# Kernel optimization log

Hardware: AMD Instinct MI355X
Metric: run time of the kernel (lower is better)

The kernel has to match this reference:

```python
import jax, jax.numpy as jnp
import numpy as np

# irreps_in = 128x0e + 64x1o + 32x2e -> (multiplicity, 2l+1) blocks
IRREPS = [(128, 1), (64, 3), (32, 5)]
DIM = sum(m * d for m, d in IRREPS)  # 480
EPS = 1e-8


def setup_inputs() -> dict:
    key = jax.random.key(0)
    features = jax.random.normal(key, (100000, DIM), dtype=jnp.float32)
    return {"features": features}


def reference(features) -> jnp.ndarray:
    batch = features.shape[:-1]
    out_blocks = []
    off = 0
    for mul, d in IRREPS:  # fixed small structural loop over irrep types
        block = features[..., off:off + mul * d].reshape(*batch, mul, d)
        # per-irrep L2 norm over the (2l+1) components -> (..., mul)
        norms = jnp.sqrt(jnp.sum(block * block, axis=-1))
        eps_norms = jnp.maximum(norms, EPS)
        scalings = jax.nn.silu(eps_norms) / eps_norms
        out_blocks.append((block * scalings[..., None]).reshape(*batch, mul * d))
        off += mul * d
    return jnp.concatenate(out_blocks, axis=-1)
```

## Files before the change

kernel.cpp:

```cpp
#include <hip/hip_runtime.h>
#include <math.h>

#define DIM 480
#define ROWS 8
#define BLOCK 64
#define NLOADS 15

typedef float f4 __attribute__((ext_vector_type(4)));

__device__ __forceinline__ float sig_of(float n) {
    n = fmaxf(n, 1e-8f);
    return __builtin_amdgcn_rcpf(1.0f + __expf(-n));
}

template <int R>
__device__ __forceinline__ void scale_groups(float* sbuf, int lane) {
    #pragma unroll
    for (int k = 0; k < R / 2; ++k) {
        const int a4 = k * 64 + lane;
        f4* p = (f4*)(sbuf + (a4 >> 5) * DIM) + (a4 & 31);
        f4 x = *p;
        x.x *= sig_of(fabsf(x.x));
        x.y *= sig_of(fabsf(x.y));
        x.z *= sig_of(fabsf(x.z));
        x.w *= sig_of(fabsf(x.w));
        *p = x;
    }
    #pragma unroll
    for (int k = 0; k < R; ++k) {
        const int b = k * 64 + lane;
        float* p = sbuf + (b >> 6) * DIM + 128 + 3 * (b & 63);
        const float x0 = p[0], x1 = p[1], x2 = p[2];
        const float s = sig_of(sqrtf(x0*x0 + x1*x1 + x2*x2));
        p[0] = x0 * s; p[1] = x1 * s; p[2] = x2 * s;
    }
    #pragma unroll
    for (int k = 0; k < R / 2; ++k) {
        const int c = k * 64 + lane;
        float* p = sbuf + (c >> 5) * DIM + 320 + 5 * (c & 31);
        const float x0 = p[0], x1 = p[1], x2 = p[2], x3 = p[3], x4 = p[4];
        const float s = sig_of(sqrtf(x0*x0 + x1*x1 + x2*x2 + x3*x3 + x4*x4));
        p[0] = x0*s; p[1] = x1*s; p[2] = x2*s; p[3] = x3*s; p[4] = x4*s;
    }
}

__device__ void scale_groups_rt(float* sbuf, int lane, int rows) {
    for (int a = lane; a < rows * 128; a += 64) {
        float* p = sbuf + (a >> 7) * DIM + (a & 127);
        const float x = *p;
        *p = x * sig_of(fabsf(x));
    }
    for (int b = lane; b < rows * 64; b += 64) {
        float* p = sbuf + (b >> 6) * DIM + 128 + 3 * (b & 63);
        const float x0 = p[0], x1 = p[1], x2 = p[2];
        const float s = sig_of(sqrtf(x0*x0 + x1*x1 + x2*x2));
        p[0] = x0 * s; p[1] = x1 * s; p[2] = x2 * s;
    }
    for (int c = lane; c < rows * 32; c += 64) {
        float* p = sbuf + (c >> 5) * DIM + 320 + 5 * (c & 31);
        const float x0 = p[0], x1 = p[1], x2 = p[2], x3 = p[3], x4 = p[4];
        const float s = sig_of(sqrtf(x0*x0 + x1*x1 + x2*x2 + x3*x3 + x4*x4));
        p[0] = x0*s; p[1] = x1*s; p[2] = x2*s; p[3] = x3*s; p[4] = x4*s;
    }
}

__global__ __launch_bounds__(BLOCK) void norm_act_kernel(
    const float* __restrict__ in, float* __restrict__ out, int n_rows)
{
    __shared__ __align__(16) float sbuf[ROWS * DIM];
    const int lane = threadIdx.x;
    const int row0 = blockIdx.x * ROWS;
    const int rows = min(ROWS, n_rows - row0);

    const float* gsrc = in  + (size_t)row0 * DIM;
    float*       gdst = out + (size_t)row0 * DIM;

    if (rows == ROWS) {
        #pragma unroll
        for (int k = 0; k < NLOADS; ++k) {
            const float* gp = gsrc + (size_t)(k * 64 + lane) * 4;
            __builtin_amdgcn_global_load_lds(
                (const __attribute__((address_space(1))) void*)gp,
                (__attribute__((address_space(3))) void*)((char*)sbuf + k * 1024),
                16, 0, 0);
        }
        asm volatile("s_waitcnt vmcnt(0)" ::: "memory");

        scale_groups<ROWS>(sbuf, lane);

        #pragma unroll
        for (int k = 0; k < NLOADS; ++k) {
            const int v = k * 64 + lane;
            __builtin_nontemporal_store(((const f4*)sbuf)[v], (f4*)gdst + v);
        }
    } else if (rows > 0) {
        for (int v = lane; v < rows * (DIM / 4); v += BLOCK)
            ((f4*)sbuf)[v] = ((const f4*)gsrc)[v];
        scale_groups_rt(sbuf, lane, rows);
        for (int v = lane; v < rows * (DIM / 4); v += BLOCK)
            __builtin_nontemporal_store(((const f4*)sbuf)[v], (f4*)gdst + v);
    }
}

extern "C" void kernel_launch(void* const* d_in, const int* in_sizes, int n_in,
                              void* d_out, int out_size, void* d_ws, size_t ws_size,
                              hipStream_t stream) {
    const float* in  = (const float*)d_in[0];
    float*       out = (float*)d_out;
    const int n_rows = in_sizes[0] / DIM;
    const int grid   = (n_rows + ROWS - 1) / ROWS;
    norm_act_kernel<<<grid, BLOCK, 0, stream>>>(in, out, n_rows);
}
```

Measured before the change: 324.2 us.

## Use persistent blocks with register double-buffered tile prefetch

Replaces the one-block-per-tile launch with a grid capped at 2560 persistent blocks. Each block walks tiles in a grid-stride loop and loads the next 8-row tile into registers while it scales and stores the current one through LDS. The aim is to keep global loads in flight during compute and stores, and to cut block launch overhead. In exchange it drops the direct global-to-LDS loads, adds about 120 VGPRs of tile buffers per thread, and adds an extra register-to-LDS copy for each tile.

```diff
diff --git a/kernel.cpp b/kernel.cpp
--- a/kernel.cpp
+++ b/kernel.cpp
@@ -4,7 +4,9 @@
 #define DIM 480
 #define ROWS 8
 #define BLOCK 64
-#define NLOADS 15
+#define NV 15
+#define TILE_F4 (ROWS * DIM / 4)
+#define NBLOCKS 2560
 
 typedef float f4 __attribute__((ext_vector_type(4)));
 
@@ -64,40 +66,66 @@
     }
 }
 
+__device__ __forceinline__ void load_tile(const f4* __restrict__ gsrc,
+                                          int lane, f4 r[NV]) {
+    #pragma unroll
+    for (int k = 0; k < NV; ++k) r[k] = gsrc[k * 64 + lane];
+}
+
+__device__ __forceinline__ void process_tile(const f4 r[NV], float* sbuf,
+                                             f4* __restrict__ gdst, int lane) {
+    #pragma unroll
+    for (int k = 0; k < NV; ++k)
+        ((f4*)sbuf)[k * 64 + lane] = r[k];
+    scale_groups<ROWS>(sbuf, lane);
+    #pragma unroll
+    for (int k = 0; k < NV; ++k)
+        __builtin_nontemporal_store(((const f4*)sbuf)[k * 64 + lane],
+                                    gdst + k * 64 + lane);
+}
+
 __global__ __launch_bounds__(BLOCK) void norm_act_kernel(
     const float* __restrict__ in, float* __restrict__ out, int n_rows)
 {
     __shared__ __align__(16) float sbuf[ROWS * DIM];
-    const int lane = threadIdx.x;
-    const int row0 = blockIdx.x * ROWS;
-    const int rows = min(ROWS, n_rows - row0);
+    const int lane   = threadIdx.x;
+    const int stride = gridDim.x;
+    const int nfull  = n_rows / ROWS;
+    const f4* gin  = (const f4*)in;
+    f4*       gout = (f4*)out;
 
-    const float* gsrc = in  + (size_t)row0 * DIM;
-    float*       gdst = out + (size_t)row0 * DIM;
+    f4 ra[NV], rb[NV];
 
-    if (rows == ROWS) {
-        #pragma unroll
-        for (int k = 0; k < NLOADS; ++k) {
-            const float* gp = gsrc + (size_t)(k * 64 + lane) * 4;
-            __builtin_amdgcn_global_load_lds(
-                (const __attribute__((address_space(1))) void*)gp,
-                (__attribute__((address_space(3))) void*)((char*)sbuf + k * 1024),
-                16, 0, 0);
+    int t = blockIdx.x;
+    if (t < nfull) {
+        load_tile(gin + (size_t)t * TILE_F4, lane, ra);
+        for (;;) {
+            const int t2 = t + stride;
+            if (t2 >= nfull) {
+                process_tile(ra, sbuf, gout + (size_t)t * TILE_F4, lane);
+                break;
+            }
+            load_tile(gin + (size_t)t2 * TILE_F4, lane, rb);
+            process_tile(ra, sbuf, gout + (size_t)t * TILE_F4, lane);
+            const int t3 = t2 + stride;
+            if (t3 >= nfull) {
+                process_tile(rb, sbuf, gout + (size_t)t2 * TILE_F4, lane);
+                break;
+            }
+            load_tile(gin + (size_t)t3 * TILE_F4, lane, ra);
+            process_tile(rb, sbuf, gout + (size_t)t2 * TILE_F4, lane);
+            t = t3;
         }
-        asm volatile("s_waitcnt vmcnt(0)" ::: "memory");
+    }
 
-        scale_groups<ROWS>(sbuf, lane);
-
-        #pragma unroll
-        for (int k = 0; k < NLOADS; ++k) {
-            const int v = k * 64 + lane;
-            __builtin_nontemporal_store(((const f4*)sbuf)[v], (f4*)gdst + v);
-        }
-    } else if (rows > 0) {
-        for (int v = lane; v < rows * (DIM / 4); v += BLOCK)
+    const int rem = n_rows - nfull * ROWS;
+    if (rem > 0 && (int)blockIdx.x == (nfull % stride)) {
+        const float* gsrc = in  + (size_t)nfull * ROWS * DIM;
+        float*       gdst = out + (size_t)nfull * ROWS * DIM;
+        for (int v = lane; v < rem * (DIM / 4); v += BLOCK)
             ((f4*)sbuf)[v] = ((const f4*)gsrc)[v];
-        scale_groups_rt(sbuf, lane, rows);
-        for (int v = lane; v < rows * (DIM / 4); v += BLOCK)
+        scale_groups_rt(sbuf, lane, rem);
+        for (int v = lane; v < rem * (DIM / 4); v += BLOCK)
             __builtin_nontemporal_store(((const f4*)sbuf)[v], (f4*)gdst + v);
     }
 }
@@ -108,6 +136,7 @@
     const float* in  = (const float*)d_in[0];
     float*       out = (float*)d_out;
     const int n_rows = in_sizes[0] / DIM;
-    const int grid   = (n_rows + ROWS - 1) / ROWS;
+    const int ntiles = (n_rows + ROWS - 1) / ROWS;
+    const int grid   = ntiles < NBLOCKS ? ntiles : NBLOCKS;
     norm_act_kernel<<<grid, BLOCK, 0, stream>>>(in, out, n_rows);
 }
```

New measurement: 333.3 us. 1.03x slower.
